# Kernel tuning notes

Measured on AMD Instinct MI355X. Metric: run time of the kernel, lower is better.

## Reference

```python
import jax, jax.numpy as jnp
import numpy as np

N, L, D = 32, 1568, 768
HEADS = 12
PART = 49
SCALE = (D // HEADS) ** (-0.5)


def setup_inputs() -> dict:
    key = jax.random.key(0)
    k1, k2, k3, k4, k5 = jax.random.split(key, 5)
    x = jax.random.normal(k1, (N, L, D), dtype=jnp.float32)
    w_qkv = jax.random.normal(k2, (3 * D, D), dtype=jnp.float32) * 0.02
    w_proj = jax.random.normal(k3, (D, D), dtype=jnp.float32) * 0.02
    b_proj = jax.random.normal(k4, (D,), dtype=jnp.float32) * 0.02
    # per-sample random permutation = argsort of uniform noise (as in source)
    noise = jax.random.uniform(k5, (N, L))
    shuffle_ids = jnp.argsort(noise, axis=-1).astype(jnp.int64)
    return {"x": x, "w_qkv": w_qkv, "w_proj": w_proj, "b_proj": b_proj,
            "shuffle_ids": shuffle_ids}


def reference(x, w_qkv, w_proj, b_proj, shuffle_ids):
    # qkv projection (no bias: qkv_bias=False)
    qkv = jnp.einsum('nld,ed->nle', x, w_qkv)          # [N, L, 3D]
    q, k, v = jnp.split(qkv, 3, axis=-1)               # each [N, L, D]
    # gather k, v by random permutation (q_shuffle=False: q not gathered)
    idx = shuffle_ids[..., None]                        # [N, L, 1]
    k = jnp.take_along_axis(k, idx, axis=1)
    v = jnp.take_along_axis(v, idx, axis=1)
    dh = D // HEADS
    # FAITHFUL to source bug: q is overwritten by k (`q = k.view(...)`)
    q = k.reshape(-1, PART, HEADS, dh)                  # [N*L/P, P, H, dh]
    kk = k.reshape(-1, PART, HEADS, dh)
    vv = v.reshape(-1, PART, HEADS, dh)
    attn = jnp.einsum('nqhd,nkhd->nqkh', q, kk) * SCALE  # [P', P, P, H]
    attn = jax.nn.softmax(attn, axis=-2)                 # softmax over k axis
    out = jnp.einsum('nqkh,nkhd->nqhd', attn, vv)        # [P', P, H, dh]
    out = out.reshape(N, L, D)  # note: left in shuffled order (q_shuffle=False)
    out = jnp.einsum('nld,ed->nle', out, w_proj) + b_proj
    return out
```

## Files before the change

kernel.cpp:

```cpp
#include <hip/hip_runtime.h>

typedef unsigned short u16;
typedef unsigned int u32;
typedef float f32x4 __attribute__((ext_vector_type(4)));
typedef __bf16 bf16x8 __attribute__((ext_vector_type(8)));

__device__ __forceinline__ u16 f2bf(float f) {
  u32 b = __float_as_uint(f);
  b += 0x7fffu + ((b >> 16) & 1u);
  return (u16)(b >> 16);
}

__device__ __forceinline__ void gload16(const void* g, void* l) {
  __builtin_amdgcn_global_load_lds(
      (const __attribute__((address_space(1))) void*)g,
      (__attribute__((address_space(3))) void*)l, 16, 0, 0);
}

__device__ __forceinline__ int xcd_swz(int wgid, int nwg) {
  const int q = nwg >> 3, r = nwg & 7;
  const int xcd = wgid & 7, pos = wgid >> 3;
  return (xcd < r ? xcd * (q + 1) : r * (q + 1) + (xcd - r) * q) + pos;
}

__global__ __launch_bounds__(256)
void cvt_f32_bf16(const float4* __restrict__ in, ushort4* __restrict__ out, int n4) {
  int i = blockIdx.x * blockDim.x + threadIdx.x;
  int stride = gridDim.x * blockDim.x;
  for (; i < n4; i += stride) {
    float4 v = in[i];
    ushort4 o;
    o.x = f2bf(v.x); o.y = f2bf(v.y); o.z = f2bf(v.z); o.w = f2bf(v.w);
    out[i] = o;
  }
}

template<bool BF16OUT>
__global__ __launch_bounds__(512, 2)
void gemm256(const u16* __restrict__ A, const u16* __restrict__ B,
             u16* __restrict__ Cb, float* __restrict__ Cf,
             const float* __restrict__ bias, int N, int K, int gx)
{
  __shared__ u16 LDS[2][4][8192];
  const int tid = threadIdx.x;
  const int lane = tid & 63;
  const int wid = tid >> 6;
  const int wm = wid >> 2, wn = wid & 3;
  const int rlo = lane & 15, g4 = lane >> 4;

  const int id = xcd_swz(blockIdx.x, gridDim.x);
  const int by = id / gx, bx = id - by * gx;
  const int row0 = by * 256, col0 = bx * 256;
  const int nk = K >> 6;

  const int sr = tid >> 3;
  const int c_phys = (tid & 7) * 16;

  auto stage = [&](int h) {
    int kt = h >> 2; if (kt > nk - 1) kt = nk - 1;
    const int type = h & 3;
    const u16* src = (type < 2) ? B : A;
    const int rbase = ((type < 2) ? col0 : row0) + (type & 1) * 128;
    const int slot = (type < 2) ? (2 + (type & 1)) : (type - 2);
    const int buf = (h >> 2) & 1;
    #pragma unroll
    for (int i = 0; i < 2; ++i) {
      int r = sr + i * 64;
      int c_log = c_phys ^ (((r >> 1) & 7) << 4);
      const u16* g = src + (size_t)(rbase + r) * K + kt * 64 + (c_log >> 1);
      gload16(g, &LDS[buf][slot][wid * 512 + i * 4096]);
    }
  };
  auto ldA = [&](int buf, int m8, int ks) -> bf16x8 {
    int row = wm * 128 + m8 * 16 + rlo;
    int r = row & 127;
    int col = (ks * 32 + g4 * 8) ^ (((r >> 1) & 7) << 3);
    return *(const bf16x8*)&LDS[buf][row >> 7][r * 64 + col];
  };
  auto ldB = [&](int buf, int n, int ks) -> bf16x8 {
    int row = wn * 64 + n * 16 + rlo;
    int r = row & 127;
    int col = (ks * 32 + g4 * 8) ^ (((r >> 1) & 7) << 3);
    return *(const bf16x8*)&LDS[buf][2 + (row >> 7)][r * 64 + col];
  };

  f32x4 acc[8][4] = {};
  bf16x8 bf[4][2], af[4][2];

  #pragma unroll
  for (int h = 0; h < 7; ++h) stage(h);
  asm volatile("s_waitcnt vmcnt(6)" ::: "memory");
  __builtin_amdgcn_s_barrier();

  for (int t = 0; t < nk; ++t) {
    const int buf = t & 1;
    #pragma unroll
    for (int n = 0; n < 4; ++n)
      #pragma unroll
      for (int ks = 0; ks < 2; ++ks) bf[n][ks] = ldB(buf, n, ks);
    #pragma unroll
    for (int m = 0; m < 4; ++m)
      #pragma unroll
      for (int ks = 0; ks < 2; ++ks) af[m][ks] = ldA(buf, m, ks);
    stage(4 * t + 7);
    __builtin_amdgcn_s_barrier();
    asm volatile("s_waitcnt lgkmcnt(0)" ::: "memory");
    __builtin_amdgcn_s_setprio(1);
    #pragma unroll
    for (int m = 0; m < 4; ++m)
      #pragma unroll
      for (int ks = 0; ks < 2; ++ks) {
        acc[m][0] = __builtin_amdgcn_mfma_f32_16x16x32_bf16(af[m][ks], bf[0][ks], acc[m][0], 0, 0, 0);
        acc[m][1] = __builtin_amdgcn_mfma_f32_16x16x32_bf16(af[m][ks], bf[1][ks], acc[m][1], 0, 0, 0);
      }
    __builtin_amdgcn_s_setprio(0);
    __builtin_amdgcn_s_barrier();
    stage(4 * t + 8);
    __builtin_amdgcn_s_barrier();
    __builtin_amdgcn_s_setprio(1);
    #pragma unroll
    for (int m = 0; m < 4; ++m)
      #pragma unroll
      for (int ks = 0; ks < 2; ++ks) {
        acc[m][2] = __builtin_amdgcn_mfma_f32_16x16x32_bf16(af[m][ks], bf[2][ks], acc[m][2], 0, 0, 0);
        acc[m][3] = __builtin_amdgcn_mfma_f32_16x16x32_bf16(af[m][ks], bf[3][ks], acc[m][3], 0, 0, 0);
      }
    __builtin_amdgcn_s_setprio(0);
    __builtin_amdgcn_s_barrier();
    #pragma unroll
    for (int m = 0; m < 4; ++m)
      #pragma unroll
      for (int ks = 0; ks < 2; ++ks) af[m][ks] = ldA(buf, 4 + m, ks);
    stage(4 * t + 9);
    __builtin_amdgcn_s_barrier();
    asm volatile("s_waitcnt lgkmcnt(0)" ::: "memory");
    __builtin_amdgcn_s_setprio(1);
    #pragma unroll
    for (int m = 0; m < 4; ++m)
      #pragma unroll
      for (int ks = 0; ks < 2; ++ks) {
        acc[4 + m][0] = __builtin_amdgcn_mfma_f32_16x16x32_bf16(af[m][ks], bf[0][ks], acc[4 + m][0], 0, 0, 0);
        acc[4 + m][1] = __builtin_amdgcn_mfma_f32_16x16x32_bf16(af[m][ks], bf[1][ks], acc[4 + m][1], 0, 0, 0);
      }
    __builtin_amdgcn_s_setprio(0);
    __builtin_amdgcn_s_barrier();
    stage(4 * t + 10);
    __builtin_amdgcn_s_barrier();
    __builtin_amdgcn_s_setprio(1);
    #pragma unroll
    for (int m = 0; m < 4; ++m)
      #pragma unroll
      for (int ks = 0; ks < 2; ++ks) {
        acc[4 + m][2] = __builtin_amdgcn_mfma_f32_16x16x32_bf16(af[m][ks], bf[2][ks], acc[4 + m][2], 0, 0, 0);
        acc[4 + m][3] = __builtin_amdgcn_mfma_f32_16x16x32_bf16(af[m][ks], bf[3][ks], acc[4 + m][3], 0, 0, 0);
      }
    __builtin_amdgcn_s_setprio(0);
    asm volatile("s_waitcnt vmcnt(6)" ::: "memory");
    __builtin_amdgcn_s_barrier();
  }

  #pragma unroll
  for (int m = 0; m < 8; ++m) {
    #pragma unroll
    for (int n = 0; n < 4; ++n) {
      int row = row0 + wm * 128 + m * 16 + g4 * 4;
      int col = col0 + wn * 64 + n * 16 + rlo;
      #pragma unroll
      for (int v = 0; v < 4; ++v) {
        if (BF16OUT) {
          Cb[(size_t)(row + v) * N + col] = f2bf(acc[m][n][v]);
        } else {
          Cf[(size_t)(row + v) * N + col] = acc[m][n][v] + bias[col];
        }
      }
    }
  }
}

__global__ __launch_bounds__(64)
void attn_part(const u16* __restrict__ kv, const int* __restrict__ ids,
               u16* __restrict__ out)
{
  __shared__ u16 Ksw[64 * 64];
  __shared__ u16 Vt[64 * 64];
  __shared__ int rowg[64];
  const int lane = threadIdx.x;
  const int p = blockIdx.x / 12;
  const int h = blockIdx.x - p * 12;
  const int n = p >> 5;
  const int lbase = (p & 31) * 49;

  if (lane < 49) rowg[lane] = n * 1568 + ids[n * 1568 + lbase + lane];
  __syncthreads();

  const int rr8 = lane >> 3, c16 = lane & 7;
  #pragma unroll
  for (int it = 0; it < 8; ++it) {
    int r = it * 8 + rr8;
    uint4 val = {0, 0, 0, 0};
    if (r < 49) val = *(const uint4*)(kv + (size_t)rowg[r] * 1536 + h * 64 + c16 * 8);
    *(uint4*)&Ksw[r * 64 + ((c16 ^ (r & 7)) * 8)] = val;
  }
  #pragma unroll
  for (int it = 0; it < 8; ++it) {
    int r = it * 8 + rr8;
    uint4 val = {0, 0, 0, 0};
    if (r < 49) val = *(const uint4*)(kv + (size_t)rowg[r] * 1536 + 768 + h * 64 + c16 * 8);
    const u16* vs = (const u16*)&val;
    #pragma unroll
    for (int j = 0; j < 8; ++j) {
      int d = c16 * 8 + j;
      Vt[d * 64 + (((r >> 3) ^ (d & 7)) * 8) + (r & 7)] = vs[j];
    }
  }
  __syncthreads();

  const int rlo = lane & 15, g4 = lane >> 4;
  bf16x8 af[4][2];
  #pragma unroll
  for (int m = 0; m < 4; ++m)
    #pragma unroll
    for (int g = 0; g < 2; ++g) {
      int row = m * 16 + rlo;
      af[m][g] = *(const bf16x8*)&Ksw[row * 64 + (((g * 4 + g4) ^ (row & 7)) * 8)];
    }
  f32x4 s[4][4] = {};
  #pragma unroll
  for (int m = 0; m < 4; ++m)
    #pragma unroll
    for (int nf = 0; nf < 4; ++nf)
      #pragma unroll
      for (int g = 0; g < 2; ++g)
        s[m][nf] = __builtin_amdgcn_mfma_f32_16x16x32_bf16(af[m][g], af[nf][g], s[m][nf], 0, 0, 0);

  #pragma unroll
  for (int m = 0; m < 4; ++m) {
    #pragma unroll
    for (int v = 0; v < 4; ++v) {
      float mx = -1e30f;
      #pragma unroll
      for (int nf = 0; nf < 4; ++nf) {
        float x = s[m][nf][v] * 0.125f;
        int col = nf * 16 + rlo;
        x = (col < 49) ? x : -1e30f;
        s[m][nf][v] = x;
        mx = fmaxf(mx, x);
      }
      #pragma unroll
      for (int d = 1; d < 16; d <<= 1) mx = fmaxf(mx, __shfl_xor(mx, d));
      float sum = 0.f;
      #pragma unroll
      for (int nf = 0; nf < 4; ++nf) {
        int col = nf * 16 + rlo;
        float e = (col < 49) ? __expf(s[m][nf][v] - mx) : 0.f;
        s[m][nf][v] = e;
        sum += e;
      }
      #pragma unroll
      for (int d = 1; d < 16; d <<= 1) sum += __shfl_xor(sum, d);
      float inv = 1.0f / sum;
      #pragma unroll
      for (int nf = 0; nf < 4; ++nf) s[m][nf][v] *= inv;
    }
  }

  __syncthreads();
  #pragma unroll
  for (int m = 0; m < 4; ++m)
    #pragma unroll
    for (int nf = 0; nf < 4; ++nf)
      #pragma unroll
      for (int v = 0; v < 4; ++v) {
        int R = m * 16 + g4 * 4 + v;
        int C = nf * 16 + rlo;
        Ksw[R * 64 + (((C >> 3) ^ (R & 7)) * 8) + (C & 7)] = f2bf(s[m][nf][v]);
      }
  __syncthreads();

  bf16x8 pa[4][2], vb[4][2];
  #pragma unroll
  for (int m = 0; m < 4; ++m)
    #pragma unroll
    for (int g = 0; g < 2; ++g) {
      int row = m * 16 + rlo;
      pa[m][g] = *(const bf16x8*)&Ksw[row * 64 + (((g * 4 + g4) ^ (row & 7)) * 8)];
    }
  #pragma unroll
  for (int nd = 0; nd < 4; ++nd)
    #pragma unroll
    for (int g = 0; g < 2; ++g) {
      int row = nd * 16 + rlo;
      vb[nd][g] = *(const bf16x8*)&Vt[row * 64 + (((g * 4 + g4) ^ (row & 7)) * 8)];
    }
  f32x4 o[4][4] = {};
  #pragma unroll
  for (int m = 0; m < 4; ++m)
    #pragma unroll
    for (int nd = 0; nd < 4; ++nd)
      #pragma unroll
      for (int g = 0; g < 2; ++g)
        o[m][nd] = __builtin_amdgcn_mfma_f32_16x16x32_bf16(pa[m][g], vb[nd][g], o[m][nd], 0, 0, 0);

  #pragma unroll
  for (int m = 0; m < 4; ++m)
    #pragma unroll
    for (int nd = 0; nd < 4; ++nd)
      #pragma unroll
      for (int v = 0; v < 4; ++v) {
        int q = m * 16 + g4 * 4 + v;
        if (q < 49) {
          size_t token = (size_t)p * 49 + q;
          out[token * 768 + h * 64 + nd * 16 + rlo] = f2bf(o[m][nd][v]);
        }
      }
}

extern "C" void kernel_launch(void* const* d_in, const int* in_sizes, int n_in,
                              void* d_out, int out_size, void* d_ws, size_t ws_size,
                              hipStream_t stream) {
  const float* x      = (const float*)d_in[0];
  const float* w_qkv  = (const float*)d_in[1];
  const float* w_proj = (const float*)d_in[2];
  const float* b_proj = (const float*)d_in[3];
  const int*   ids    = (const int*)d_in[4];
  float* outp = (float*)d_out;

  char* ws = (char*)d_ws;
  u16* kvbuf = (u16*)ws;
  u16* xbuf  = (u16*)(ws + 154140672);
  u16* wkv   = (u16*)(ws + 154140672 + 77070336);
  u16* wproj = (u16*)(ws + 154140672 + 77070336 + 2359296);

  auto cgrid = [](int n4) { int g = (n4 + 255) / 256; return g > 2048 ? 2048 : g; };

  cvt_f32_bf16<<<cgrid(9633792), 256, 0, stream>>>((const float4*)x, (ushort4*)xbuf, 9633792);
  cvt_f32_bf16<<<cgrid(294912), 256, 0, stream>>>((const float4*)(w_qkv + 768 * 768), (ushort4*)wkv, 294912);
  cvt_f32_bf16<<<cgrid(147456), 256, 0, stream>>>((const float4*)w_proj, (ushort4*)wproj, 147456);

  gemm256<true><<<dim3(6 * 196), 512, 0, stream>>>(xbuf, wkv, kvbuf, nullptr, nullptr, 1536, 768, 6);

  attn_part<<<12288, 64, 0, stream>>>(kvbuf, ids, xbuf);

  gemm256<false><<<dim3(3 * 196), 512, 0, stream>>>(xbuf, wproj, nullptr, outp, b_proj, 768, 768, 3);
}
```

Before: 574.4 us.

## Scatter KV rows by inverse permutation in GEMM epilogue; deepen staging prefetch

A small kernel builds the inverse of each sample's shuffle permutation. The KV projection GEMM uses it to write each output row directly to its shuffled position, so the attention kernel reads 49 consecutive rows instead of gathering them through an index table. The GEMM prologue also stages one more tile and issues two stages per phase, keeping more loads in flight. The cost is scattered row stores in the epilogue, an extra small launch and extra workspace for the inverse table.

```diff
diff --git a/kernel.cpp b/kernel.cpp
--- a/kernel.cpp
+++ b/kernel.cpp
@@ -35,11 +35,21 @@
   }
 }
 
+__global__ __launch_bounds__(256)
+void inv_perm(const int* __restrict__ ids, int* __restrict__ inv, int total, int L) {
+  int i = blockIdx.x * 256 + threadIdx.x;
+  if (i < total) {
+    int n = i / L, l = i - n * L;
+    inv[n * L + ids[i]] = l;
+  }
+}
+
 template<bool BF16OUT>
 __global__ __launch_bounds__(512, 2)
 void gemm256(const u16* __restrict__ A, const u16* __restrict__ B,
              u16* __restrict__ Cb, float* __restrict__ Cf,
-             const float* __restrict__ bias, int N, int K, int gx)
+             const float* __restrict__ bias, const int* __restrict__ scat,
+             int N, int K, int gx)
 {
   __shared__ u16 LDS[2][4][8192];
   const int tid = threadIdx.x;
@@ -61,7 +71,7 @@
     const int type = h & 3;
     const u16* src = (type < 2) ? B : A;
     const int rbase = ((type < 2) ? col0 : row0) + (type & 1) * 128;
-    const int slot = (type < 2) ? (2 + (type & 1)) : (type - 2);
+    const int slot = (type < 2) ? (2 + type) : (type - 2);
     const int buf = (h >> 2) & 1;
     #pragma unroll
     for (int i = 0; i < 2; ++i) {
@@ -88,8 +98,8 @@
   bf16x8 bf[4][2], af[4][2];
 
   #pragma unroll
-  for (int h = 0; h < 7; ++h) stage(h);
-  asm volatile("s_waitcnt vmcnt(6)" ::: "memory");
+  for (int h = 0; h < 8; ++h) stage(h);
+  asm volatile("s_waitcnt vmcnt(8)" ::: "memory");
   __builtin_amdgcn_s_barrier();
 
   for (int t = 0; t < nk; ++t) {
@@ -102,7 +112,6 @@
     for (int m = 0; m < 4; ++m)
       #pragma unroll
       for (int ks = 0; ks < 2; ++ks) af[m][ks] = ldA(buf, m, ks);
-    stage(4 * t + 7);
     __builtin_amdgcn_s_barrier();
     asm volatile("s_waitcnt lgkmcnt(0)" ::: "memory");
     __builtin_amdgcn_s_setprio(1);
@@ -116,6 +125,7 @@
     __builtin_amdgcn_s_setprio(0);
     __builtin_amdgcn_s_barrier();
     stage(4 * t + 8);
+    stage(4 * t + 9);
     __builtin_amdgcn_s_barrier();
     __builtin_amdgcn_s_setprio(1);
     #pragma unroll
@@ -131,7 +141,6 @@
     for (int m = 0; m < 4; ++m)
       #pragma unroll
       for (int ks = 0; ks < 2; ++ks) af[m][ks] = ldA(buf, 4 + m, ks);
-    stage(4 * t + 9);
     __builtin_amdgcn_s_barrier();
     asm volatile("s_waitcnt lgkmcnt(0)" ::: "memory");
     __builtin_amdgcn_s_setprio(1);
@@ -145,6 +154,7 @@
     __builtin_amdgcn_s_setprio(0);
     __builtin_amdgcn_s_barrier();
     stage(4 * t + 10);
+    stage(4 * t + 11);
     __builtin_amdgcn_s_barrier();
     __builtin_amdgcn_s_setprio(1);
     #pragma unroll
@@ -155,7 +165,7 @@
         acc[4 + m][3] = __builtin_amdgcn_mfma_f32_16x16x32_bf16(af[m][ks], bf[3][ks], acc[4 + m][3], 0, 0, 0);
       }
     __builtin_amdgcn_s_setprio(0);
-    asm volatile("s_waitcnt vmcnt(6)" ::: "memory");
+    asm volatile("s_waitcnt vmcnt(8)" ::: "memory");
     __builtin_amdgcn_s_barrier();
   }
 
@@ -168,7 +178,10 @@
       #pragma unroll
       for (int v = 0; v < 4; ++v) {
         if (BF16OUT) {
-          Cb[(size_t)(row + v) * N + col] = f2bf(acc[m][n][v]);
+          int d = row + v;
+          int nn = d / 1568;
+          int dest = nn * 1568 + scat[d];
+          Cb[(size_t)dest * N + col] = f2bf(acc[m][n][v]);
         } else {
           Cf[(size_t)(row + v) * N + col] = acc[m][n][v] + bias[col];
         }
@@ -178,34 +191,28 @@
 }
 
 __global__ __launch_bounds__(64)
-void attn_part(const u16* __restrict__ kv, const int* __restrict__ ids,
-               u16* __restrict__ out)
+void attn_part(const u16* __restrict__ kv, u16* __restrict__ out)
 {
   __shared__ u16 Ksw[64 * 64];
   __shared__ u16 Vt[64 * 64];
-  __shared__ int rowg[64];
   const int lane = threadIdx.x;
   const int p = blockIdx.x / 12;
   const int h = blockIdx.x - p * 12;
-  const int n = p >> 5;
-  const int lbase = (p & 31) * 49;
-
-  if (lane < 49) rowg[lane] = n * 1568 + ids[n * 1568 + lbase + lane];
-  __syncthreads();
+  const u16* kbase = kv + (size_t)p * 49 * 1536 + h * 64;
 
   const int rr8 = lane >> 3, c16 = lane & 7;
   #pragma unroll
   for (int it = 0; it < 8; ++it) {
     int r = it * 8 + rr8;
     uint4 val = {0, 0, 0, 0};
-    if (r < 49) val = *(const uint4*)(kv + (size_t)rowg[r] * 1536 + h * 64 + c16 * 8);
+    if (r < 49) val = *(const uint4*)(kbase + (size_t)r * 1536 + c16 * 8);
     *(uint4*)&Ksw[r * 64 + ((c16 ^ (r & 7)) * 8)] = val;
   }
   #pragma unroll
   for (int it = 0; it < 8; ++it) {
     int r = it * 8 + rr8;
     uint4 val = {0, 0, 0, 0};
-    if (r < 49) val = *(const uint4*)(kv + (size_t)rowg[r] * 1536 + 768 + h * 64 + c16 * 8);
+    if (r < 49) val = *(const uint4*)(kbase + (size_t)r * 1536 + 768 + c16 * 8);
     const u16* vs = (const u16*)&val;
     #pragma unroll
     for (int j = 0; j < 8; ++j) {
@@ -330,16 +337,18 @@
   u16* xbuf  = (u16*)(ws + 154140672);
   u16* wkv   = (u16*)(ws + 154140672 + 77070336);
   u16* wproj = (u16*)(ws + 154140672 + 77070336 + 2359296);
+  int* invp  = (int*)(ws + 154140672 + 77070336 + 2359296 + 1179648);
 
   auto cgrid = [](int n4) { int g = (n4 + 255) / 256; return g > 2048 ? 2048 : g; };
 
   cvt_f32_bf16<<<cgrid(9633792), 256, 0, stream>>>((const float4*)x, (ushort4*)xbuf, 9633792);
   cvt_f32_bf16<<<cgrid(294912), 256, 0, stream>>>((const float4*)(w_qkv + 768 * 768), (ushort4*)wkv, 294912);
   cvt_f32_bf16<<<cgrid(147456), 256, 0, stream>>>((const float4*)w_proj, (ushort4*)wproj, 147456);
-
-  gemm256<true><<<dim3(6 * 196), 512, 0, stream>>>(xbuf, wkv, kvbuf, nullptr, nullptr, 1536, 768, 6);
-
-  attn_part<<<12288, 64, 0, stream>>>(kvbuf, ids, xbuf);
-
-  gemm256<false><<<dim3(3 * 196), 512, 0, stream>>>(xbuf, wproj, nullptr, outp, b_proj, 768, 768, 3);
-}
+  inv_perm<<<196, 256, 0, stream>>>(ids, invp, 50176, 1568);
+
+  gemm256<true><<<dim3(6 * 196), 512, 0, stream>>>(xbuf, wkv, kvbuf, nullptr, nullptr, invp, 1536, 768, 6);
+
+  attn_part<<<12288, 64, 0, stream>>>(kvbuf, xbuf);
+
+  gemm256<false><<<dim3(3 * 196), 512, 0, stream>>>(xbuf, wproj, nullptr, outp, b_proj, nullptr, 768, 768, 3);
+}
```

Result: no change. 581.9 us (+1.3%).
